# Kernel optimization log

Hardware: AMD Instinct MI355X
Metric: run time of the kernel (lower is better)

## Reference

```python
import jax, jax.numpy as jnp
import numpy as np

OUT_H = 7
OUT_W = 7
SPATIAL_SCALE = 0.25
SAMPLE_NUM = 2  # sampling grid per bin is SAMPLE_NUM x SAMPLE_NUM


def setup_inputs() -> dict:
    key = jax.random.key(0)
    k1, k2, k3, k4, k5, k6, k7 = jax.random.split(key, 7)
    B, C, H, W = 4, 256, 256, 256
    N = 1000
    features = jax.random.normal(k1, (B, C, H, W), dtype=jnp.float32)
    img_h = H / SPATIAL_SCALE
    img_w = W / SPATIAL_SCALE
    bidx = jax.random.randint(k2, (N,), 0, B).astype(jnp.float32)
    cx = jax.random.uniform(k3, (N,), minval=0.0, maxval=img_w)
    cy = jax.random.uniform(k4, (N,), minval=0.0, maxval=img_h)
    w = jax.random.uniform(k5, (N,), minval=16.0, maxval=256.0)
    h = jax.random.uniform(k6, (N,), minval=16.0, maxval=256.0)
    theta = jax.random.uniform(k7, (N,), minval=-np.pi, maxval=np.pi)
    rois = jnp.stack([bidx, cx, cy, w, h, theta], axis=1)  # [N,6]
    return {"features": features, "rois": rois}


def _rroi_align(features, rois):
    B, C, H, W = features.shape
    N = rois.shape[0]
    S = SAMPLE_NUM
    f32 = jnp.float32

    bidx = rois[:, 0].astype(jnp.int32)
    cx = rois[:, 1] * SPATIAL_SCALE
    cy = rois[:, 2] * SPATIAL_SCALE
    rw = jnp.maximum(rois[:, 3] * SPATIAL_SCALE, 0.0)
    rh = jnp.maximum(rois[:, 4] * SPATIAL_SCALE, 0.0)
    theta = rois[:, 5]

    bin_h = rh / OUT_H  # [N]
    bin_w = rw / OUT_W

    ph = jnp.arange(OUT_H, dtype=f32)
    pw = jnp.arange(OUT_W, dtype=f32)
    s = (jnp.arange(S, dtype=f32) + 0.5) / S  # sub-bin offsets

    # local (un-rotated) sample coords relative to roi center
    # yy: [N, PH, Sy], xx: [N, PW, Sx]
    yy = bin_h[:, None, None] * (ph[None, :, None] + s[None, None, :]) - rh[:, None, None] * 0.5
    xx = bin_w[:, None, None] * (pw[None, :, None] + s[None, None, :]) - rw[:, None, None] * 0.5
    # broadcast to [N, PH, PW, Sy, Sx]
    yy = yy[:, :, None, :, None]
    xx = xx[:, None, :, None, :]
    cosT = jnp.cos(theta)[:, None, None, None, None]
    sinT = jnp.sin(theta)[:, None, None, None, None]

    # rotate into feature-map coords (matches RRoIAlign CUDA kernel)
    x = xx * cosT + yy * sinT + cx[:, None, None, None, None]
    y = yy * cosT - xx * sinT + cy[:, None, None, None, None]

    # bilinear interpolation with out-of-bounds -> 0 (kernel semantics)
    valid = (y > -1.0) & (y < H) & (x > -1.0) & (x < W)
    yc = jnp.clip(y, 0.0, H - 1.0)
    xc = jnp.clip(x, 0.0, W - 1.0)
    y0 = jnp.clip(jnp.floor(yc), 0.0, H - 2.0).astype(jnp.int32)
    x0 = jnp.clip(jnp.floor(xc), 0.0, W - 2.0).astype(jnp.int32)
    y1 = y0 + 1
    x1 = x0 + 1
    ly = yc - y0.astype(f32)
    lx = xc - x0.astype(f32)
    hy = 1.0 - ly
    hx = 1.0 - lx

    b = bidx[:, None, None, None, None]

    def gather(yi, xi):
        # -> [N, PH, PW, Sy, Sx, C]
        return features[b, :, yi, xi]

    w00 = (hy * hx * valid)[..., None]
    w01 = (hy * lx * valid)[..., None]
    w10 = (ly * hx * valid)[..., None]
    w11 = (ly * lx * valid)[..., None]

    val = (w00 * gather(y0, x0) + w01 * gather(y0, x1)
           + w10 * gather(y1, x0) + w11 * gather(y1, x1))
    # average over the S*S sampling grid -> [N, PH, PW, C]
    out = val.sum(axis=(3, 4)) / float(S * S)
    return jnp.transpose(out, (0, 3, 1, 2))  # [N, C, PH, PW]


def reference(features, rois):
    return _rroi_align(features, rois)
```

## Files before the change

kernel.cpp:

```cpp
#include <hip/hip_runtime.h>

#define OUT_H 7
#define OUT_W 7
#define NBINS (OUT_H * OUT_W)
#define NSAMP (NBINS * 2 * 2)
#define CCH 256
#define FH 256
#define FW 256
#define HW (FH * FW)
#define CHW (CCH * HW)
#define SCALE 0.25f

__device__ __forceinline__ unsigned int f2bf(float f) {
    unsigned int u = __float_as_uint(f);
    u += 0x7FFFu + ((u >> 16) & 1u);
    return u >> 16;
}
#define BFLO(u) __uint_as_float((u) << 16)
#define BFHI(u) __uint_as_float((u) & 0xFFFF0000u)

__global__ __launch_bounds__(256) void transpose_kernel(
    const float* __restrict__ feat, unsigned int* __restrict__ featT)
{
    __shared__ float tile[64][65];
    const int t  = threadIdx.x;
    const int s0 = blockIdx.x * 64;
    const int c0 = blockIdx.y * 64;
    const int b  = blockIdx.z;

    const float* inb = feat + (size_t)b * CHW + (size_t)c0 * HW + s0;

    const int rx = (t & 15) * 4;
    const int rc = t >> 4;
    #pragma unroll
    for (int pass = 0; pass < 4; ++pass) {
        int c = pass * 16 + rc;
        float4 v = *(const float4*)(inb + (size_t)c * HW + rx);
        tile[c][rx]     = v.x;
        tile[c][rx + 1] = v.y;
        tile[c][rx + 2] = v.z;
        tile[c][rx + 3] = v.w;
    }
    __syncthreads();

    unsigned int* outb = featT + (size_t)b * (HW * 128) + (size_t)s0 * 128 + (c0 >> 1);
    const int p  = t & 7;
    const int r0 = t >> 3;
    #pragma unroll
    for (int pass = 0; pass < 2; ++pass) {
        int r = pass * 32 + r0;
        unsigned int u0 = f2bf(tile[p * 8 + 0][r]) | (f2bf(tile[p * 8 + 1][r]) << 16);
        unsigned int u1 = f2bf(tile[p * 8 + 2][r]) | (f2bf(tile[p * 8 + 3][r]) << 16);
        unsigned int u2 = f2bf(tile[p * 8 + 4][r]) | (f2bf(tile[p * 8 + 5][r]) << 16);
        unsigned int u3 = f2bf(tile[p * 8 + 6][r]) | (f2bf(tile[p * 8 + 7][r]) << 16);
        *(uint4*)(outb + (size_t)r * 128 + p * 4) = make_uint4(u0, u1, u2, u3);
    }
}

__global__ __launch_bounds__(512) void gather_kernel(
    const unsigned short* __restrict__ featT,
    const float* __restrict__ rois,
    float* __restrict__ out)
{
    const int n = blockIdx.x;
    const int t = threadIdx.x;

    __shared__ int   s_off[NSAMP];
    __shared__ float s_w[4][NSAMP];
    __shared__ float s_out[NBINS][260];

    const float* rr = rois + (size_t)n * 6;

    if (t < NSAMP) {
        float cx = rr[1] * SCALE, cy = rr[2] * SCALE;
        float rw = fmaxf(rr[3] * SCALE, 0.f), rh = fmaxf(rr[4] * SCALE, 0.f);
        float theta = rr[5];
        float bin_h = rh * (1.f / OUT_H), bin_w = rw * (1.f / OUT_W);

        int sx = t & 1, sy = (t >> 1) & 1, pp = t >> 2;
        int pw = pp % OUT_W, ph = pp / OUT_W;

        float yy = bin_h * ((float)ph + ((float)sy + 0.5f) * 0.5f) - rh * 0.5f;
        float xx = bin_w * ((float)pw + ((float)sx + 0.5f) * 0.5f) - rw * 0.5f;
        float ct = cosf(theta), st = sinf(theta);
        float x = xx * ct + yy * st + cx;
        float y = yy * ct - xx * st + cy;

        float v = (y > -1.f && y < (float)FH && x > -1.f && x < (float)FW) ? 0.25f : 0.f;
        float ycl = fminf(fmaxf(y, 0.f), (float)(FH - 1));
        float xcl = fminf(fmaxf(x, 0.f), (float)(FW - 1));
        float y0f = fminf(fmaxf(floorf(ycl), 0.f), (float)(FH - 2));
        float x0f = fminf(fmaxf(floorf(xcl), 0.f), (float)(FW - 2));
        int y0 = (int)y0f, x0 = (int)x0f;
        float ly = ycl - y0f, lx = xcl - x0f;
        float hy = 1.f - ly, hx = 1.f - lx;

        s_off[t] = ((int)rr[0]) * HW + y0 * FW + x0;
        s_w[0][t] = hy * hx * v;
        s_w[1][t] = hy * lx * v;
        s_w[2][t] = ly * hx * v;
        s_w[3][t] = ly * lx * v;
    }
    __syncthreads();

    const int lane = t & 63;
    const int w    = t >> 6;
    const int cl   = lane >> 1;
    const int half = lane & 1;

    for (int pp = w; pp < NBINS; pp += 8) {
        float a0=0.f,a1=0.f,a2=0.f,a3=0.f,a4=0.f,a5=0.f,a6=0.f,a7=0.f;
        #pragma unroll
        for (int k = 0; k < 4; ++k) {
            int sid = pp * 4 + k;
            size_t base = (size_t)s_off[sid] * 256 + 8 * cl + 256 * half;
            float wa = s_w[half][sid];
            float wb = s_w[2 + half][sid];
            uint4 va = *(const uint4*)(featT + base);
            uint4 vb = *(const uint4*)(featT + base + 256 * FW);
            a0 += wa * BFLO(va.x) + wb * BFLO(vb.x);
            a1 += wa * BFHI(va.x) + wb * BFHI(vb.x);
            a2 += wa * BFLO(va.y) + wb * BFLO(vb.y);
            a3 += wa * BFHI(va.y) + wb * BFHI(vb.y);
            a4 += wa * BFLO(va.z) + wb * BFLO(vb.z);
            a5 += wa * BFHI(va.z) + wb * BFHI(vb.z);
            a6 += wa * BFLO(va.w) + wb * BFLO(vb.w);
            a7 += wa * BFHI(va.w) + wb * BFHI(vb.w);
        }
        a0 += __shfl_xor(a0, 1); a1 += __shfl_xor(a1, 1);
        a2 += __shfl_xor(a2, 1); a3 += __shfl_xor(a3, 1);
        a4 += __shfl_xor(a4, 1); a5 += __shfl_xor(a5, 1);
        a6 += __shfl_xor(a6, 1); a7 += __shfl_xor(a7, 1);

        float4 r = half ? make_float4(a4, a5, a6, a7)
                        : make_float4(a0, a1, a2, a3);
        *(float4*)&s_out[pp][4 * lane] = r;
    }
    __syncthreads();

    float* o = out + (size_t)n * (CCH * NBINS);
    for (int g = t; g < CCH * NBINS; g += 512) {
        int c  = g / NBINS;
        int pp = g - c * NBINS;
        o[g] = s_out[pp][c];
    }
}

__global__ __launch_bounds__(1024) void sort_rois_kernel(
    const float* __restrict__ rois, int N, int* __restrict__ perm)
{
    __shared__ int s_key[1024];
    __shared__ int s_val[1024];
    const int t = threadIdx.x;

    int key = 0x7FFFFFFF, val = 0;
    if (t < N) {
        const float* r = rois + (size_t)t * 6;
        int bi = (int)r[0];
        int cyb = min(15, max(0, (int)(r[2] * SCALE * (1.f / 16.f))));
        int cxb = min(15, max(0, (int)(r[1] * SCALE * (1.f / 16.f))));
        key = (bi << 18) | (cyb << 14) | (cxb << 10) | t;
        val = t;
    }
    s_key[t] = key; s_val[t] = val;
    __syncthreads();

    for (int k = 2; k <= 1024; k <<= 1) {
        for (int j = k >> 1; j > 0; j >>= 1) {
            int ixj = t ^ j;
            if (ixj > t) {
                int a = s_key[t], bkey = s_key[ixj];
                bool up = ((t & k) == 0);
                if ((a > bkey) == up) {
                    s_key[t] = bkey; s_key[ixj] = a;
                    int av = s_val[t]; s_val[t] = s_val[ixj]; s_val[ixj] = av;
                }
            }
            __syncthreads();
        }
    }
    if (t < N) perm[t] = s_val[t];
}

__global__ __launch_bounds__(256) void rroi_align_fallback(
    const float* __restrict__ feat,
    const float* __restrict__ rois,
    const int* __restrict__ perm,
    int N, int P,
    float* __restrict__ out)
{
    const int b   = blockIdx.x;
    const int xcd = b & 7;
    const int s   = b >> 3;
    const int gy  = s / P;
    const int rl  = s - gy * P;
    const int r   = xcd * P + rl;
    if (r >= N) return;
    const int n = perm ? perm[r] : r;
    const int t = threadIdx.x;

    __shared__ int   s_off[NSAMP];
    __shared__ float s_w0[NSAMP], s_w1[NSAMP], s_w2[NSAMP], s_w3[NSAMP];
    __shared__ int   s_b;

    const float* rr = rois + (size_t)n * 6;

    if (t < NSAMP) {
        float cx = rr[1] * SCALE, cy = rr[2] * SCALE;
        float rw = fmaxf(rr[3] * SCALE, 0.f), rh = fmaxf(rr[4] * SCALE, 0.f);
        float theta = rr[5];
        float bin_h = rh * (1.f / OUT_H), bin_w = rw * (1.f / OUT_W);

        int sx = t & 1, sy = (t >> 1) & 1, pp = t >> 2;
        int pw = pp % OUT_W, ph = pp / OUT_W;

        float yy = bin_h * ((float)ph + ((float)sy + 0.5f) * 0.5f) - rh * 0.5f;
        float xx = bin_w * ((float)pw + ((float)sx + 0.5f) * 0.5f) - rw * 0.5f;
        float ct = cosf(theta), st = sinf(theta);
        float x = xx * ct + yy * st + cx;
        float y = yy * ct - xx * st + cy;

        float v = (y > -1.f && y < (float)FH && x > -1.f && x < (float)FW) ? 0.25f : 0.f;
        float ycl = fminf(fmaxf(y, 0.f), (float)(FH - 1));
        float xcl = fminf(fmaxf(x, 0.f), (float)(FW - 1));
        float y0f = fminf(fmaxf(floorf(ycl), 0.f), (float)(FH - 2));
        float x0f = fminf(fmaxf(floorf(xcl), 0.f), (float)(FW - 2));
        int y0 = (int)y0f, x0 = (int)x0f;
        float ly = ycl - y0f, lx = xcl - x0f;
        float hy = 1.f - ly, hx = 1.f - lx;

        s_off[t] = y0 * FW + x0;
        s_w0[t] = hy * hx * v;
        s_w1[t] = hy * lx * v;
        s_w2[t] = ly * hx * v;
        s_w3[t] = ly * lx * v;
        if (t == 0) s_b = (int)rr[0];
    }
    __syncthreads();

    const float* fb = feat + (size_t)s_b * CHW;

    #pragma unroll
    for (int i = 0; i < 7; ++i) {
        int flat = (gy * 7 + i) * 256 + t;
        int c  = flat / 49;
        int pp = flat - c * 49;
        const float* fc = fb + (size_t)c * HW;

        float acc = 0.f;
        #pragma unroll
        for (int k = 0; k < 4; ++k) {
            int sid = pp * 4 + k;
            const float* p = fc + s_off[sid];
            acc += s_w0[sid] * p[0]  + s_w1[sid] * p[1]
                 + s_w2[sid] * p[FW] + s_w3[sid] * p[FW + 1];
        }
        out[(size_t)n * (CCH * OUT_H * OUT_W) + flat] = acc;
    }
}

extern "C" void kernel_launch(void* const* d_in, const int* in_sizes, int n_in,
                              void* d_out, int out_size, void* d_ws, size_t ws_size,
                              hipStream_t stream)
{
    const float* feat = (const float*)d_in[0];
    const float* rois = (const float*)d_in[1];
    float* out = (float*)d_out;
    int N = in_sizes[1] / 6;
    int B = in_sizes[0] / CHW;

    const size_t needT = (size_t)B * HW * CCH * 2;

    if (ws_size >= needT) {
        unsigned int* featT = (unsigned int*)d_ws;
        dim3 tg(HW / 64, CCH / 64, B);
        transpose_kernel<<<tg, 256, 0, stream>>>(feat, featT);
        gather_kernel<<<N, 512, 0, stream>>>((const unsigned short*)d_ws, rois, out);
    } else if (ws_size >= 4096 && N <= 1024) {
        int* perm = (int*)d_ws;
        sort_rois_kernel<<<1, 1024, 0, stream>>>(rois, N, perm);
        int P  = (N + 7) / 8;
        int NB = 8 * P * 7;
        rroi_align_fallback<<<NB, 256, 0, stream>>>(feat, rois, perm, N, P, out);
    } else {
        int P  = (N + 7) / 8;
        int NB = 8 * P * 7;
        rroi_align_fallback<<<NB, 256, 0, stream>>>(feat, rois, (const int*)nullptr, N, P, out);
    }
}
```

Measured before the change: 128.5 us.

## Sort ROIs spatially, split channels across blocks with XCD-aware mapping, nontemporal I/O

Adds a spatial sort of ROIs ahead of the bf16 transpose+gather path. The gather grid now maps blocks to XCDs so that spatially nearby ROIs share an L2, and each ROI is split into two 128-channel half-blocks of 256 threads. The transpose uses nontemporal loads and the output is written with vectorized nontemporal stores from a channel-major shared buffer. The goal is better L2 reuse of gathered feature rows and less cache pollution from streaming traffic. In exchange it adds a sort kernel launch, requires 4KB more workspace, and doubles the per-ROI weight setup across the two half-blocks.

After: 132.1 us. 2.8% more time.

```diff
diff --git a/kernel.cpp b/kernel.cpp
--- a/kernel.cpp
+++ b/kernel.cpp
@@ -11,6 +11,8 @@
 #define CHW (CCH * HW)
 #define SCALE 0.25f
 
+typedef float v4f __attribute__((ext_vector_type(4)));
+
 __device__ __forceinline__ unsigned int f2bf(float f) {
     unsigned int u = __float_as_uint(f);
     u += 0x7FFFu + ((u >> 16) & 1u);
@@ -18,133 +20,6 @@
 }
 #define BFLO(u) __uint_as_float((u) << 16)
 #define BFHI(u) __uint_as_float((u) & 0xFFFF0000u)
-
-__global__ __launch_bounds__(256) void transpose_kernel(
-    const float* __restrict__ feat, unsigned int* __restrict__ featT)
-{
-    __shared__ float tile[64][65];
-    const int t  = threadIdx.x;
-    const int s0 = blockIdx.x * 64;
-    const int c0 = blockIdx.y * 64;
-    const int b  = blockIdx.z;
-
-    const float* inb = feat + (size_t)b * CHW + (size_t)c0 * HW + s0;
-
-    const int rx = (t & 15) * 4;
-    const int rc = t >> 4;
-    #pragma unroll
-    for (int pass = 0; pass < 4; ++pass) {
-        int c = pass * 16 + rc;
-        float4 v = *(const float4*)(inb + (size_t)c * HW + rx);
-        tile[c][rx]     = v.x;
-        tile[c][rx + 1] = v.y;
-        tile[c][rx + 2] = v.z;
-        tile[c][rx + 3] = v.w;
-    }
-    __syncthreads();
-
-    unsigned int* outb = featT + (size_t)b * (HW * 128) + (size_t)s0 * 128 + (c0 >> 1);
-    const int p  = t & 7;
-    const int r0 = t >> 3;
-    #pragma unroll
-    for (int pass = 0; pass < 2; ++pass) {
-        int r = pass * 32 + r0;
-        unsigned int u0 = f2bf(tile[p * 8 + 0][r]) | (f2bf(tile[p * 8 + 1][r]) << 16);
-        unsigned int u1 = f2bf(tile[p * 8 + 2][r]) | (f2bf(tile[p * 8 + 3][r]) << 16);
-        unsigned int u2 = f2bf(tile[p * 8 + 4][r]) | (f2bf(tile[p * 8 + 5][r]) << 16);
-        unsigned int u3 = f2bf(tile[p * 8 + 6][r]) | (f2bf(tile[p * 8 + 7][r]) << 16);
-        *(uint4*)(outb + (size_t)r * 128 + p * 4) = make_uint4(u0, u1, u2, u3);
-    }
-}
-
-__global__ __launch_bounds__(512) void gather_kernel(
-    const unsigned short* __restrict__ featT,
-    const float* __restrict__ rois,
-    float* __restrict__ out)
-{
-    const int n = blockIdx.x;
-    const int t = threadIdx.x;
-
-    __shared__ int   s_off[NSAMP];
-    __shared__ float s_w[4][NSAMP];
-    __shared__ float s_out[NBINS][260];
-
-    const float* rr = rois + (size_t)n * 6;
-
-    if (t < NSAMP) {
-        float cx = rr[1] * SCALE, cy = rr[2] * SCALE;
-        float rw = fmaxf(rr[3] * SCALE, 0.f), rh = fmaxf(rr[4] * SCALE, 0.f);
-        float theta = rr[5];
-        float bin_h = rh * (1.f / OUT_H), bin_w = rw * (1.f / OUT_W);
-
-        int sx = t & 1, sy = (t >> 1) & 1, pp = t >> 2;
-        int pw = pp % OUT_W, ph = pp / OUT_W;
-
-        float yy = bin_h * ((float)ph + ((float)sy + 0.5f) * 0.5f) - rh * 0.5f;
-        float xx = bin_w * ((float)pw + ((float)sx + 0.5f) * 0.5f) - rw * 0.5f;
-        float ct = cosf(theta), st = sinf(theta);
-        float x = xx * ct + yy * st + cx;
-        float y = yy * ct - xx * st + cy;
-
-        float v = (y > -1.f && y < (float)FH && x > -1.f && x < (float)FW) ? 0.25f : 0.f;
-        float ycl = fminf(fmaxf(y, 0.f), (float)(FH - 1));
-        float xcl = fminf(fmaxf(x, 0.f), (float)(FW - 1));
-        float y0f = fminf(fmaxf(floorf(ycl), 0.f), (float)(FH - 2));
-        float x0f = fminf(fmaxf(floorf(xcl), 0.f), (float)(FW - 2));
-        int y0 = (int)y0f, x0 = (int)x0f;
-        float ly = ycl - y0f, lx = xcl - x0f;
-        float hy = 1.f - ly, hx = 1.f - lx;
-
-        s_off[t] = ((int)rr[0]) * HW + y0 * FW + x0;
-        s_w[0][t] = hy * hx * v;
-        s_w[1][t] = hy * lx * v;
-        s_w[2][t] = ly * hx * v;
-        s_w[3][t] = ly * lx * v;
-    }
-    __syncthreads();
-
-    const int lane = t & 63;
-    const int w    = t >> 6;
-    const int cl   = lane >> 1;
-    const int half = lane & 1;
-
-    for (int pp = w; pp < NBINS; pp += 8) {
-        float a0=0.f,a1=0.f,a2=0.f,a3=0.f,a4=0.f,a5=0.f,a6=0.f,a7=0.f;
-        #pragma unroll
-        for (int k = 0; k < 4; ++k) {
-            int sid = pp * 4 + k;
-            size_t base = (size_t)s_off[sid] * 256 + 8 * cl + 256 * half;
-            float wa = s_w[half][sid];
-            float wb = s_w[2 + half][sid];
-            uint4 va = *(const uint4*)(featT + base);
-            uint4 vb = *(const uint4*)(featT + base + 256 * FW);
-            a0 += wa * BFLO(va.x) + wb * BFLO(vb.x);
-            a1 += wa * BFHI(va.x) + wb * BFHI(vb.x);
-            a2 += wa * BFLO(va.y) + wb * BFLO(vb.y);
-            a3 += wa * BFHI(va.y) + wb * BFHI(vb.y);
-            a4 += wa * BFLO(va.z) + wb * BFLO(vb.z);
-            a5 += wa * BFHI(va.z) + wb * BFHI(vb.z);
-            a6 += wa * BFLO(va.w) + wb * BFLO(vb.w);
-            a7 += wa * BFHI(va.w) + wb * BFHI(vb.w);
-        }
-        a0 += __shfl_xor(a0, 1); a1 += __shfl_xor(a1, 1);
-        a2 += __shfl_xor(a2, 1); a3 += __shfl_xor(a3, 1);
-        a4 += __shfl_xor(a4, 1); a5 += __shfl_xor(a5, 1);
-        a6 += __shfl_xor(a6, 1); a7 += __shfl_xor(a7, 1);
-
-        float4 r = half ? make_float4(a4, a5, a6, a7)
-                        : make_float4(a0, a1, a2, a3);
-        *(float4*)&s_out[pp][4 * lane] = r;
-    }
-    __syncthreads();
-
-    float* o = out + (size_t)n * (CCH * NBINS);
-    for (int g = t; g < CCH * NBINS; g += 512) {
-        int c  = g / NBINS;
-        int pp = g - c * NBINS;
-        o[g] = s_out[pp][c];
-    }
-}
 
 __global__ __launch_bounds__(1024) void sort_rois_kernel(
     const float* __restrict__ rois, int N, int* __restrict__ perm)
@@ -182,6 +57,137 @@
     if (t < N) perm[t] = s_val[t];
 }
 
+__global__ __launch_bounds__(256) void transpose_kernel(
+    const float* __restrict__ feat, unsigned int* __restrict__ featT)
+{
+    __shared__ float tile[64][65];
+    const int t  = threadIdx.x;
+    const int s0 = blockIdx.x * 64;
+    const int c0 = blockIdx.y * 64;
+    const int b  = blockIdx.z;
+
+    const float* inb = feat + (size_t)b * CHW + (size_t)c0 * HW + s0;
+
+    const int rx = (t & 15) * 4;
+    const int rc = t >> 4;
+    #pragma unroll
+    for (int pass = 0; pass < 4; ++pass) {
+        int c = pass * 16 + rc;
+        v4f v = __builtin_nontemporal_load((const v4f*)(inb + (size_t)c * HW + rx));
+        tile[c][rx]     = v.x;
+        tile[c][rx + 1] = v.y;
+        tile[c][rx + 2] = v.z;
+        tile[c][rx + 3] = v.w;
+    }
+    __syncthreads();
+
+    unsigned int* outb = featT + (size_t)b * (HW * 128) + (size_t)s0 * 128 + (c0 >> 1);
+    const int p  = t & 7;
+    const int r0 = t >> 3;
+    #pragma unroll
+    for (int pass = 0; pass < 2; ++pass) {
+        int r = pass * 32 + r0;
+        unsigned int u0 = f2bf(tile[p * 8 + 0][r]) | (f2bf(tile[p * 8 + 1][r]) << 16);
+        unsigned int u1 = f2bf(tile[p * 8 + 2][r]) | (f2bf(tile[p * 8 + 3][r]) << 16);
+        unsigned int u2 = f2bf(tile[p * 8 + 4][r]) | (f2bf(tile[p * 8 + 5][r]) << 16);
+        unsigned int u3 = f2bf(tile[p * 8 + 6][r]) | (f2bf(tile[p * 8 + 7][r]) << 16);
+        *(uint4*)(outb + (size_t)r * 128 + p * 4) = make_uint4(u0, u1, u2, u3);
+    }
+}
+
+__global__ __launch_bounds__(256) void gather_kernel(
+    const unsigned short* __restrict__ featT,
+    const float* __restrict__ rois,
+    const int* __restrict__ perm,
+    int N, int P,
+    float* __restrict__ out)
+{
+    const int b   = blockIdx.x;
+    const int xcd = b & 7;
+    const int i   = b >> 3;
+    const int ri  = xcd * P + (i >> 1);
+    const int gy  = i & 1;
+    if (ri >= N) return;
+    const int n = perm ? perm[ri] : ri;
+    const int t = threadIdx.x;
+
+    __shared__ int   s_off[NSAMP];
+    __shared__ float s_w[4][NSAMP];
+    __shared__ float s_out[128 * NBINS];
+
+    const float* rr = rois + (size_t)n * 6;
+
+    if (t < NSAMP) {
+        float cx = rr[1] * SCALE, cy = rr[2] * SCALE;
+        float rw = fmaxf(rr[3] * SCALE, 0.f), rh = fmaxf(rr[4] * SCALE, 0.f);
+        float theta = rr[5];
+        float bin_h = rh * (1.f / OUT_H), bin_w = rw * (1.f / OUT_W);
+
+        int sx = t & 1, sy = (t >> 1) & 1, pp = t >> 2;
+        int pw = pp % OUT_W, ph = pp / OUT_W;
+
+        float yy = bin_h * ((float)ph + ((float)sy + 0.5f) * 0.5f) - rh * 0.5f;
+        float xx = bin_w * ((float)pw + ((float)sx + 0.5f) * 0.5f) - rw * 0.5f;
+        float ct = cosf(theta), st = sinf(theta);
+        float x = xx * ct + yy * st + cx;
+        float y = yy * ct - xx * st + cy;
+
+        float v = (y > -1.f && y < (float)FH && x > -1.f && x < (float)FW) ? 0.25f : 0.f;
+        float ycl = fminf(fmaxf(y, 0.f), (float)(FH - 1));
+        float xcl = fminf(fmaxf(x, 0.f), (float)(FW - 1));
+        float y0f = fminf(fmaxf(floorf(ycl), 0.f), (float)(FH - 2));
+        float x0f = fminf(fmaxf(floorf(xcl), 0.f), (float)(FW - 2));
+        int y0 = (int)y0f, x0 = (int)x0f;
+        float ly = ycl - y0f, lx = xcl - x0f;
+        float hy = 1.f - ly, hx = 1.f - lx;
+
+        s_off[t] = ((int)rr[0]) * HW + y0 * FW + x0;
+        s_w[0][t] = hy * hx * v;
+        s_w[1][t] = hy * lx * v;
+        s_w[2][t] = ly * hx * v;
+        s_w[3][t] = ly * lx * v;
+    }
+    __syncthreads();
+
+    const int lane = t & 63;
+    const int w    = t >> 6;
+    const int quad = lane >> 1;
+    const int half = lane & 1;
+    const int cbase = gy * 128 + 4 * quad;
+
+    #pragma unroll 2
+    for (int pp = w; pp < NBINS; pp += 4) {
+        float a0 = 0.f, a1 = 0.f, a2 = 0.f, a3 = 0.f;
+        #pragma unroll
+        for (int k = 0; k < 4; ++k) {
+            int sid = pp * 4 + k;
+            size_t base = (size_t)s_off[sid] * 256 + 256 * half + cbase;
+            float wa = s_w[half][sid];
+            float wb = s_w[2 + half][sid];
+            uint2 va = *(const uint2*)(featT + base);
+            uint2 vb = *(const uint2*)(featT + base + 256 * FW);
+            a0 += wa * BFLO(va.x) + wb * BFLO(vb.x);
+            a1 += wa * BFHI(va.x) + wb * BFHI(vb.x);
+            a2 += wa * BFLO(va.y) + wb * BFLO(vb.y);
+            a3 += wa * BFHI(va.y) + wb * BFHI(vb.y);
+        }
+        a0 += __shfl_xor(a0, 1); a1 += __shfl_xor(a1, 1);
+        a2 += __shfl_xor(a2, 1); a3 += __shfl_xor(a3, 1);
+
+        float lo = half ? a2 : a0;
+        float hi = half ? a3 : a1;
+        s_out[(2 * lane) * NBINS + pp]     = lo;
+        s_out[(2 * lane + 1) * NBINS + pp] = hi;
+    }
+    __syncthreads();
+
+    float* o = out + (size_t)n * (CCH * NBINS) + (size_t)gy * (128 * NBINS);
+    for (int g4 = t; g4 < (128 * NBINS) / 4; g4 += 256) {
+        v4f r = *(const v4f*)(s_out + 4 * g4);
+        __builtin_nontemporal_store(r, (v4f*)(o + 4 * g4));
+    }
+}
+
 __global__ __launch_bounds__(256) void rroi_align_fallback(
     const float* __restrict__ feat,
     const float* __restrict__ rois,
@@ -268,22 +274,28 @@
     float* out = (float*)d_out;
     int N = in_sizes[1] / 6;
     int B = in_sizes[0] / CHW;
+    int P = (N + 7) / 8;
 
     const size_t needT = (size_t)B * HW * CCH * 2;
 
-    if (ws_size >= needT) {
+    if (ws_size >= needT + 4096) {
         unsigned int* featT = (unsigned int*)d_ws;
+        int* perm = (int*)((char*)d_ws + needT);
+        const int* permArg = nullptr;
+        if (N <= 1024) {
+            sort_rois_kernel<<<1, 1024, 0, stream>>>(rois, N, perm);
+            permArg = perm;
+        }
         dim3 tg(HW / 64, CCH / 64, B);
         transpose_kernel<<<tg, 256, 0, stream>>>(feat, featT);
-        gather_kernel<<<N, 512, 0, stream>>>((const unsigned short*)d_ws, rois, out);
+        gather_kernel<<<8 * P * 2, 256, 0, stream>>>(
+            (const unsigned short*)featT, rois, permArg, N, P, out);
     } else if (ws_size >= 4096 && N <= 1024) {
         int* perm = (int*)d_ws;
         sort_rois_kernel<<<1, 1024, 0, stream>>>(rois, N, perm);
-        int P  = (N + 7) / 8;
         int NB = 8 * P * 7;
         rroi_align_fallback<<<NB, 256, 0, stream>>>(feat, rois, perm, N, P, out);
     } else {
-        int P  = (N + 7) / 8;
         int NB = 8 * P * 7;
         rroi_align_fallback<<<NB, 256, 0, stream>>>(feat, rois, (const int*)nullptr, N, P, out);
     }
```
